# Kernel tuning notes

Hardware: AMD Instinct MI355X
Metric: run time of the kernel (lower is better)

The kernel has to match this reference:

```python
import jax, jax.numpy as jnp
import numpy as np

H = 1024
V = 32000
L = 15
B = 512


def setup_inputs() -> dict:
    key = jax.random.key(0)
    ks = jax.random.split(key, 16)
    s = 0.02
    return {
        "input_ids": jax.random.randint(ks[0], (B,), 0, V),
        "hidden": jax.random.normal(ks[1], (1, B, H), jnp.float32),
        "encoder_outputs": jax.random.normal(ks[2], (L, B, H), jnp.float32),
        "max_length": L,
        "embedding": jax.random.normal(ks[3], (V, H), jnp.float32) * s,
        "attn1_w": jax.random.normal(ks[4], (1, 2 * H), jnp.float32) * s,
        "attn1_b": jnp.zeros((1,), jnp.float32),
        "combine_w": jax.random.normal(ks[5], (H, 2 * H), jnp.float32) * s,
        "combine_b": jnp.zeros((H,), jnp.float32),
        "w_ih": jax.random.normal(ks[6], (3 * H, H), jnp.float32) * s,
        "w_hh": jax.random.normal(ks[7], (3 * H, H), jnp.float32) * s,
        "b_ih": jnp.zeros((3 * H,), jnp.float32),
        "b_hh": jnp.zeros((3 * H,), jnp.float32),
        "out_w": jax.random.normal(ks[8], (V, H), jnp.float32) * s,
        "out_b": jnp.zeros((V,), jnp.float32),
    }


def reference(input_ids, hidden, encoder_outputs, max_length, embedding,
              attn1_w, attn1_b, combine_w, combine_b,
              w_ih, w_hh, b_ih, b_hh, out_w, out_b):
    # embedding lookup (dropout is identity in eval mode)
    emb = embedding[input_ids]                       # [B, H]
    # Bahdanau-style additive scores: vectorize the per-step python loop
    emb_l = jnp.broadcast_to(emb[None], (max_length, B, H))   # [L, B, H]
    cat = jnp.concatenate([emb_l, encoder_outputs], axis=-1)  # [L, B, 2H]
    scores = cat @ attn1_w.T + attn1_b               # [L, B, 1]
    attn_weights = jax.nn.softmax(scores, axis=0)    # softmax over L
    ctx = jnp.sum(attn_weights * encoder_outputs, axis=0)     # [B, H]
    x = jnp.concatenate([emb, ctx], axis=-1) @ combine_w.T + combine_b  # [B, H]
    # n_layers = 1: relu then one GRU step (seq len 1)
    x = jax.nn.relu(x)
    h = hidden[0]                                    # [B, H]
    gi = x @ w_ih.T + b_ih                           # [B, 3H]
    gh = h @ w_hh.T + b_hh                           # [B, 3H]
    i_r, i_z, i_n = jnp.split(gi, 3, axis=1)
    h_r, h_z, h_n = jnp.split(gh, 3, axis=1)
    r = jax.nn.sigmoid(i_r + h_r)
    z = jax.nn.sigmoid(i_z + h_z)
    n = jnp.tanh(i_n + r * h_n)
    h_new = (1.0 - z) * n + z * h                    # [B, H]
    logits = h_new @ out_w.T + out_b                 # [B, V]
    output = jax.nn.log_softmax(logits, axis=1)
    return output, h_new[None], attn_weights
```

## Files before the change

kernel.cpp:

```cpp
#include <hip/hip_runtime.h>

#define HH 1024
#define VV 32000
#define LL 15
#define BB 512

typedef __bf16 bf16;
typedef __bf16 bf16x4 __attribute__((ext_vector_type(4)));
typedef __bf16 bf16x8 __attribute__((ext_vector_type(8)));
typedef float f32x4 __attribute__((ext_vector_type(4)));

__device__ __forceinline__ unsigned short f2bf(float f) {
    unsigned int u = __float_as_uint(f);
    unsigned int r = (u + 0x7fffu + ((u >> 16) & 1u)) >> 16;
    return (unsigned short)r;
}

__device__ __forceinline__ void gld_lds16(const void* g, void* l) {
    __builtin_amdgcn_global_load_lds(
        (const __attribute__((address_space(1))) unsigned int*)g,
        (__attribute__((address_space(3))) unsigned int*)l, 16, 0, 0);
}

__global__ __launch_bounds__(256)
void cvt4_kernel(const float* __restrict__ a0, unsigned short* __restrict__ o0, int n0_,
                 const float* __restrict__ a1, unsigned short* __restrict__ o1, int n1_,
                 const float* __restrict__ a2, unsigned short* __restrict__ o2, int n2_,
                 const float* __restrict__ a3, unsigned short* __restrict__ o3, int n3_) {
    int i = blockIdx.x * 256 + threadIdx.x;
    const float* src; unsigned short* dst;
    if (i < n0_) { src = a0; dst = o0; }
    else if ((i -= n0_) < n1_) { src = a1; dst = o1; }
    else if ((i -= n1_) < n2_) { src = a2; dst = o2; }
    else if ((i -= n2_) < n3_) { src = a3; dst = o3; }
    else return;
    const f32x4 a = ((const f32x4*)src)[2 * i], b = ((const f32x4*)src)[2 * i + 1];
    ((bf16x4*)dst)[2 * i]     = __builtin_convertvector(a, bf16x4);
    ((bf16x4*)dst)[2 * i + 1] = __builtin_convertvector(b, bf16x4);
}

__global__ __launch_bounds__(256)
void attn_kernel(const int* __restrict__ ids, const float* __restrict__ enc,
                 const float* __restrict__ embedding,
                 const float* __restrict__ attn1_w, const float* __restrict__ attn1_b,
                 float* __restrict__ attn_out, unsigned short* __restrict__ cat_out) {
    const int b = blockIdx.x, tid = threadIdx.x;
    const int lane = tid & 63, wv = tid >> 6;

    __shared__ float s_enc[LL * HH];
    __shared__ float s_scores[LL];
    __shared__ float s_red[4];

    for (int idx = tid; idx < LL * HH / 4; idx += 256) {
        const int l = (idx * 4) >> 10, h = (idx * 4) & (HH - 1);
        *(f32x4*)&s_enc[idx * 4] = *(const f32x4*)&enc[((size_t)l * BB + b) * HH + h];
    }

    const float* embr = embedding + (size_t)ids[b] * HH;
    float p = 0.f;
    for (int j = tid; j < HH; j += 256) p += embr[j] * attn1_w[j];
    #pragma unroll
    for (int o = 32; o; o >>= 1) p += __shfl_xor(p, o);
    if (lane == 0) s_red[wv] = p;
    __syncthreads();
    const float semb = s_red[0] + s_red[1] + s_red[2] + s_red[3] + attn1_b[0];

    for (int l = wv; l < LL; l += 4) {
        float q = 0.f;
        for (int j = lane; j < HH; j += 64) q += s_enc[l * HH + j] * attn1_w[HH + j];
        #pragma unroll
        for (int o = 32; o; o >>= 1) q += __shfl_xor(q, o);
        if (lane == 0) s_scores[l] = q + semb;
    }
    __syncthreads();

    float mx = -3.4e38f;
    #pragma unroll
    for (int l = 0; l < LL; l++) mx = fmaxf(mx, s_scores[l]);
    float aw[LL], sum = 0.f;
    #pragma unroll
    for (int l = 0; l < LL; l++) { aw[l] = __expf(s_scores[l] - mx); sum += aw[l]; }
    const float inv = 1.f / sum;
    #pragma unroll
    for (int l = 0; l < LL; l++) aw[l] *= inv;

    if (tid < LL) attn_out[tid * BB + b] = aw[tid];

    for (int j = tid; j < HH; j += 256) {
        float c = 0.f;
        #pragma unroll
        for (int l = 0; l < LL; l++) c += aw[l] * s_enc[l * HH + j];
        cat_out[(size_t)b * (2 * HH) + j] = f2bf(embr[j]);
        cat_out[(size_t)b * (2 * HH) + HH + j] = f2bf(c);
    }
}

template<int TM, int TN, int OUT, int GATES>
__global__ __launch_bounds__(256)
void gemm_nt(const bf16* __restrict__ A, const bf16* __restrict__ B,
             const float* __restrict__ bias, void* __restrict__ Cout,
             const bf16* __restrict__ A2, const bf16* __restrict__ B2,
             const float* __restrict__ bias2, void* __restrict__ C2,
             const int K, const int N) {
    constexpr int FM = TM / 32, FN = TN / 32;
    __shared__ bf16 As[2][TM * 64];
    __shared__ bf16 Bs[2][TN * 64];

    if (GATES && blockIdx.z == 1) { A = A2; B = B2; bias = bias2; Cout = C2; }

    const int tid = threadIdx.x;
    const int lane = tid & 63, wave = tid >> 6;
    const int wm = wave >> 1, wn = wave & 1;
    const int rlo = lane & 15, khi = lane >> 4;
    const int m0 = blockIdx.y * TM, n0 = blockIdx.x * TN;

    f32x4 acc[FM][FN] = {};
    constexpr int IA = TM / 32, IB = TN / 32;

    auto stage = [&](int k0, int buf) {
        #pragma unroll
        for (int i = 0; i < IA; i++) {
            const int p = (i * 256 + tid) * 16;
            const int row = p >> 7;
            const int qs = (p & 127) ^ ((row & 7) << 4);
            gld_lds16(A + (size_t)(m0 + row) * K + k0 + (qs >> 1),
                      &As[buf][0] + i * 2048 + wave * 512);
        }
        #pragma unroll
        for (int i = 0; i < IB; i++) {
            const int p = (i * 256 + tid) * 16;
            const int row = p >> 7;
            const int qs = (p & 127) ^ ((row & 7) << 4);
            gld_lds16(B + (size_t)(n0 + row) * K + k0 + (qs >> 1),
                      &Bs[buf][0] + i * 2048 + wave * 512);
        }
    };

    auto compute = [&](int buf) {
        #pragma unroll
        for (int ks = 0; ks < 2; ks++) {
            bf16x8 af[FM], bfr[FN];
            #pragma unroll
            for (int m = 0; m < FM; m++) {
                const int r = wm * (TM / 2) + m * 16 + rlo;
                const int sw = (ks * 64 + khi * 16) ^ ((r & 7) << 4);
                af[m] = *(const bf16x8*)((const char*)&As[buf][0] + r * 128 + sw);
            }
            #pragma unroll
            for (int n = 0; n < FN; n++) {
                const int r = wn * (TN / 2) + n * 16 + rlo;
                const int sw = (ks * 64 + khi * 16) ^ ((r & 7) << 4);
                bfr[n] = *(const bf16x8*)((const char*)&Bs[buf][0] + r * 128 + sw);
            }
            #pragma unroll
            for (int m = 0; m < FM; m++)
                #pragma unroll
                for (int n = 0; n < FN; n++)
                    acc[m][n] = __builtin_amdgcn_mfma_f32_16x16x32_bf16(af[m], bfr[n], acc[m][n], 0, 0, 0);
        }
    };

    stage(0, 0);
    __syncthreads();
    int cur = 0;
    const int NT = K >> 6;
    for (int kt = 0; kt < NT; kt++) {
        if (kt + 1 < NT) stage((kt + 1) << 6, cur ^ 1);
        compute(cur);
        __syncthreads();
        cur ^= 1;
    }

    #pragma unroll
    for (int m = 0; m < FM; m++) {
        const int gr = m0 + wm * (TM / 2) + m * 16 + khi * 4;
        #pragma unroll
        for (int n = 0; n < FN; n++) {
            const int gc = n0 + wn * (TN / 2) + n * 16 + rlo;
            const float bv = bias[gc];
            #pragma unroll
            for (int j = 0; j < 4; j++) {
                float v = acc[m][n][j] + bv;
                if (OUT == 1) {
                    v = fmaxf(v, 0.f);
                    ((unsigned short*)Cout)[(size_t)(gr + j) * N + gc] = f2bf(v);
                } else {
                    ((float*)Cout)[(size_t)(gr + j) * N + gc] = v;
                }
            }
        }
    }
}

__global__ __launch_bounds__(256, 3)
void gemm_out(const bf16* __restrict__ A, const float* __restrict__ B,
              const float* __restrict__ bias, float* __restrict__ C,
              float* __restrict__ pmax, float* __restrict__ psum) {
    constexpr int K = HH, N = VV;
    __shared__ bf16 As[2][128 * 64];
    __shared__ bf16 Bs[2][64 * 64];
    __shared__ float sPm[2][128], sPs[2][128];

    const int tid = threadIdx.x;
    const int lane = tid & 63, wave = tid >> 6;
    const int wm = wave >> 1, wn = wave & 1;
    const int rlo = lane & 15, khi = lane >> 4;

    constexpr int gridN = VV / 64;
    constexpr int nFull = (gridN >> 3) << 5;
    const int bidx = blockIdx.x;
    int g, jm;
    if (bidx < nFull) { const int s = bidx >> 5, rem = bidx & 31; jm = rem >> 3; g = s * 8 + (rem & 7); }
    else { const int rem = bidx - nFull; constexpr int gleft = gridN & 7; g = (gridN & ~7) + rem % gleft; jm = rem / gleft; }
    const int n0 = g * 64, m0 = jm * 128;

    f32x4 acc[4][2] = {};
    f32x4 bvA[4], bvB[4];

    auto loadB = [&](int k0, f32x4* bv) {
        #pragma unroll
        for (int i = 0; i < 4; i++) {
            const int idx = i * 256 + tid;
            const int row = idx >> 4, c4 = idx & 15;
            bv[i] = *(const f32x4*)(B + (size_t)(n0 + row) * K + k0 + c4 * 4);
        }
    };
    auto stageA = [&](int k0, int buf) {
        #pragma unroll
        for (int i = 0; i < 4; i++) {
            const int p = (i * 256 + tid) * 16;
            const int row = p >> 7;
            const int qs = (p & 127) ^ ((row & 7) << 4);
            gld_lds16(A + (size_t)(m0 + row) * K + k0 + (qs >> 1),
                      &As[buf][0] + i * 2048 + wave * 512);
        }
    };
    auto writeB = [&](const f32x4* bv, int buf) {
        #pragma unroll
        for (int i = 0; i < 4; i++) {
            const int idx = i * 256 + tid;
            const int row = idx >> 4, c4 = idx & 15;
            bf16x4 w = __builtin_convertvector(bv[i], bf16x4);
            *(bf16x4*)((char*)&Bs[buf][0] + row * 128 + ((c4 * 8) ^ ((row & 7) << 4))) = w;
        }
    };
    auto compute = [&](int buf) {
        #pragma unroll
        for (int ks = 0; ks < 2; ks++) {
            bf16x8 af[4], bfr[2];
            #pragma unroll
            for (int m = 0; m < 4; m++) {
                const int r = wm * 64 + m * 16 + rlo;
                const int sw = (ks * 64 + khi * 16) ^ ((r & 7) << 4);
                af[m] = *(const bf16x8*)((const char*)&As[buf][0] + r * 128 + sw);
            }
            #pragma unroll
            for (int n = 0; n < 2; n++) {
                const int r = wn * 32 + n * 16 + rlo;
                const int sw = (ks * 64 + khi * 16) ^ ((r & 7) << 4);
                bfr[n] = *(const bf16x8*)((const char*)&Bs[buf][0] + r * 128 + sw);
            }
            #pragma unroll
            for (int m = 0; m < 4; m++)
                #pragma unroll
                for (int n = 0; n < 2; n++)
                    acc[m][n] = __builtin_amdgcn_mfma_f32_16x16x32_bf16(af[m], bfr[n], acc[m][n], 0, 0, 0);
        }
    };

    loadB(0, bvA);
    stageA(0, 0);
    writeB(bvA, 0);
    loadB(64, bvA);
    __syncthreads();

    int cur = 0;
    for (int kt = 0; kt < 16; kt += 2) {
        {
            const int k1 = (kt + 1) << 6, k2 = (kt + 2) << 6;
            if (k1 < K) stageA(k1, cur ^ 1);
            if (k2 < K) loadB(k2, bvB);
            compute(cur);
            if (k1 < K) writeB(bvA, cur ^ 1);
            __syncthreads();
            cur ^= 1;
        }
        {
            const int k2 = (kt + 2) << 6, k3 = (kt + 3) << 6;
            if (k2 < K) stageA(k2, cur ^ 1);
            if (k3 < K) loadB(k3, bvA);
            compute(cur);
            if (k2 < K) writeB(bvB, cur ^ 1);
            __syncthreads();
            cur ^= 1;
        }
    }

    float bvn[2];
    #pragma unroll
    for (int n = 0; n < 2; n++) bvn[n] = bias[n0 + wn * 32 + n * 16 + rlo];

    #pragma unroll
    for (int m = 0; m < 4; m++) {
        const int rbase = wm * 64 + m * 16 + khi * 4;
        #pragma unroll
        for (int j = 0; j < 4; j++) {
            const int gr = m0 + rbase + j;
            float v[2];
            #pragma unroll
            for (int n = 0; n < 2; n++) {
                v[n] = acc[m][n][j] + bvn[n];
                C[(size_t)gr * N + n0 + wn * 32 + n * 16 + rlo] = v[n];
            }
            float lm = fmaxf(v[0], v[1]);
            #pragma unroll
            for (int o = 8; o; o >>= 1) lm = fmaxf(lm, __shfl_xor(lm, o));
            float ls = __expf(v[0] - lm) + __expf(v[1] - lm);
            #pragma unroll
            for (int o = 8; o; o >>= 1) ls += __shfl_xor(ls, o);
            if (rlo == 0) { sPm[wn][rbase + j] = lm; sPs[wn][rbase + j] = ls; }
        }
    }
    __syncthreads();
    if (tid < 128) {
        const float ma = sPm[0][tid], mb = sPm[1][tid];
        const float M = fmaxf(ma, mb);
        const float S = sPs[0][tid] * __expf(ma - M) + sPs[1][tid] * __expf(mb - M);
        pmax[(size_t)(m0 + tid) * 512 + g] = M;
        psum[(size_t)(m0 + tid) * 512 + g] = S;
    }
}

__global__ __launch_bounds__(256)
void gru_kernel(const float* __restrict__ gi, const float* __restrict__ gh,
                const float* __restrict__ h, float* __restrict__ hnew,
                unsigned short* __restrict__ hnew_bf) {
    const int i = blockIdx.x * 256 + threadIdx.x;
    const int e = i * 4;
    const int b = e >> 10, j = e & (HH - 1);
    const size_t o = ((size_t)b * 3 * HH + j) / 4;
    const f32x4 ir = ((const f32x4*)gi)[o],          iz = ((const f32x4*)gi)[o + HH / 4],
                in_ = ((const f32x4*)gi)[o + 2 * HH / 4];
    const f32x4 hr = ((const f32x4*)gh)[o],          hz = ((const f32x4*)gh)[o + HH / 4],
                hn = ((const f32x4*)gh)[o + 2 * HH / 4];
    const f32x4 hv = ((const f32x4*)h)[i];
    f32x4 out;
    ushort4 ob;
    #pragma unroll
    for (int c = 0; c < 4; c++) {
        const float r = 1.f / (1.f + __expf(-(ir[c] + hr[c])));
        const float z = 1.f / (1.f + __expf(-(iz[c] + hz[c])));
        const float n = tanhf(in_[c] + r * hn[c]);
        const float v = (1.f - z) * n + z * hv[c];
        out[c] = v;
        ((unsigned short*)&ob)[c] = f2bf(v);
    }
    ((f32x4*)hnew)[i] = out;
    ((ushort4*)hnew_bf)[i] = ob;
}

__global__ __launch_bounds__(512)
void lsm_final(const float* __restrict__ pmax, const float* __restrict__ psum,
               float* __restrict__ logits) {
    const int b = blockIdx.x, tid = threadIdx.x;
    const int lane = tid & 63, wv = tid >> 6;
    __shared__ float sm[8], ss[8];

    float m = -3.4e38f, s = 0.f;
    if (tid < VV / 64) { m = pmax[(size_t)b * 512 + tid]; s = psum[(size_t)b * 512 + tid]; }
    #pragma unroll
    for (int o = 32; o; o >>= 1) {
        const float mo = __shfl_xor(m, o), so = __shfl_xor(s, o);
        const float nm = fmaxf(m, mo);
        s = s * __expf(m - nm) + so * __expf(mo - nm);
        m = nm;
    }
    if (lane == 0) { sm[wv] = m; ss[wv] = s; }
    __syncthreads();
    float M = sm[0], S;
    #pragma unroll
    for (int w = 1; w < 8; w++) M = fmaxf(M, sm[w]);
    S = ss[0] * __expf(sm[0] - M);
    #pragma unroll
    for (int w = 1; w < 8; w++) S += ss[w] * __expf(sm[w] - M);
    const float lse = M + __logf(S);

    float* row = logits + (size_t)b * VV;
    for (int j = tid; j < VV / 4; j += 512) {
        f32x4 v = ((const f32x4*)row)[j];
        v[0] -= lse; v[1] -= lse; v[2] -= lse; v[3] -= lse;
        ((f32x4*)row)[j] = v;
    }
}

extern "C" void kernel_launch(void* const* d_in, const int* in_sizes, int n_in,
                              void* d_out, int out_size, void* d_ws, size_t ws_size,
                              hipStream_t stream) {
    const int*   ids       = (const int*)d_in[0];
    const float* hidden    = (const float*)d_in[1];
    const float* enc       = (const float*)d_in[2];
    const float* embedding = (const float*)d_in[4];
    const float* attn1_w   = (const float*)d_in[5];
    const float* attn1_b   = (const float*)d_in[6];
    const float* combine_w = (const float*)d_in[7];
    const float* combine_b = (const float*)d_in[8];
    const float* w_ih      = (const float*)d_in[9];
    const float* w_hh      = (const float*)d_in[10];
    const float* b_ih      = (const float*)d_in[11];
    const float* b_hh      = (const float*)d_in[12];
    const float* out_w     = (const float*)d_in[13];
    const float* out_b     = (const float*)d_in[14];

    float* out_lsm = (float*)d_out;
    float* out_h   = out_lsm + (size_t)BB * VV;
    float* out_aw  = out_h + (size_t)BB * HH;

    char* w = (char*)d_ws;
    unsigned short* w_ih_bf  = (unsigned short*)w;   w += (size_t)3 * HH * HH * 2;
    unsigned short* w_hh_bf  = (unsigned short*)w;   w += (size_t)3 * HH * HH * 2;
    unsigned short* w_cb_bf  = (unsigned short*)w;   w += (size_t)2 * HH * HH * 2;
    unsigned short* cat_bf   = (unsigned short*)w;   w += (size_t)BB * 2 * HH * 2;
    unsigned short* x_bf     = (unsigned short*)w;   w += (size_t)BB * HH * 2;
    unsigned short* hid_bf   = (unsigned short*)w;   w += (size_t)BB * HH * 2;
    unsigned short* hnew_bf  = (unsigned short*)w;   w += (size_t)BB * HH * 2;
    float* gi   = (float*)w;                         w += (size_t)BB * 3 * HH * 4;
    float* gh   = (float*)w;                         w += (size_t)BB * 3 * HH * 4;
    float* pmax = (float*)w;                         w += (size_t)BB * 512 * 4;
    float* psum = (float*)w;                         w += (size_t)BB * 512 * 4;

    cvt4_kernel<<<(3 * HH * HH / 8 * 2 + 2 * HH * HH / 8 + BB * HH / 8) / 256, 256, 0, stream>>>(
        w_ih, w_ih_bf, 3 * HH * HH / 8,
        w_hh, w_hh_bf, 3 * HH * HH / 8,
        combine_w, w_cb_bf, 2 * HH * HH / 8,
        hidden, hid_bf, BB * HH / 8);

    attn_kernel<<<BB, 256, 0, stream>>>(ids, enc, embedding, attn1_w, attn1_b, out_aw, cat_bf);

    gemm_nt<64, 64, 1, 0><<<dim3(HH / 64, BB / 64), 256, 0, stream>>>(
        (const bf16*)cat_bf, (const bf16*)w_cb_bf, combine_b, x_bf,
        nullptr, nullptr, nullptr, nullptr, 2 * HH, HH);

    gemm_nt<64, 64, 0, 1><<<dim3(3 * HH / 64, BB / 64, 2), 256, 0, stream>>>(
        (const bf16*)hid_bf, (const bf16*)w_hh_bf, b_hh, gh,
        (const bf16*)x_bf, (const bf16*)w_ih_bf, b_ih, gi, HH, 3 * HH);

    gru_kernel<<<(BB * HH / 4) / 256, 256, 0, stream>>>(gi, gh, hidden, out_h, hnew_bf);

    gemm_out<<<(VV / 64) * 4, 256, 0, stream>>>(
        (const bf16*)hnew_bf, out_w, out_b, out_lsm, pmax, psum);

    lsm_final<<<BB, 512, 0, stream>>>(pmax, psum, out_lsm);
}
```

Baseline: 183.8 us.

## Use explicit vmcnt waits and raw barriers for deeper double-buffered GEMM pipelining

Both GEMM kernels replace __syncthreads-based double buffering with a two-stage prefetch. Stage k+2 is issued right after the compute on stage k, and the code waits with explicit s_waitcnt vmcnt counts plus raw s_barrier and sched_barrier fences. This lets global-to-LDS loads stay in flight across compute instead of draining every iteration. The risk is correctness and hazards: the vmcnt values must match exactly the number of outstanding loads per thread, and the loop now assumes an even tile count.

```diff
diff --git a/kernel.cpp b/kernel.cpp
--- a/kernel.cpp
+++ b/kernel.cpp
@@ -9,6 +9,11 @@
 typedef __bf16 bf16x4 __attribute__((ext_vector_type(4)));
 typedef __bf16 bf16x8 __attribute__((ext_vector_type(8)));
 typedef float f32x4 __attribute__((ext_vector_type(4)));
+
+#define VMCNT(n) asm volatile("s_waitcnt vmcnt(" #n ")" ::: "memory")
+#define LGKM0    asm volatile("s_waitcnt lgkmcnt(0)" ::: "memory")
+#define SBAR     __builtin_amdgcn_s_barrier()
+#define SCHED0   __builtin_amdgcn_sched_barrier(0)
 
 __device__ __forceinline__ unsigned short f2bf(float f) {
     unsigned int u = __float_as_uint(f);
@@ -160,15 +165,27 @@
         }
     };
 
+    const int NT = K >> 6;
     stage(0, 0);
-    __syncthreads();
-    int cur = 0;
-    const int NT = K >> 6;
-    for (int kt = 0; kt < NT; kt++) {
-        if (kt + 1 < NT) stage((kt + 1) << 6, cur ^ 1);
-        compute(cur);
-        __syncthreads();
-        cur ^= 1;
+    stage(64, 1);
+
+    for (int kt = 0; kt < NT; kt += 2) {
+        {
+            const int t = kt;
+            if (t + 1 < NT) { VMCNT(4); } else { VMCNT(0); }
+            SCHED0; SBAR; SCHED0;
+            compute(0);
+            SCHED0; SBAR; SCHED0;
+            if (t + 2 < NT) stage((t + 2) << 6, 0);
+        }
+        {
+            const int t = kt + 1;
+            if (t + 1 < NT) { VMCNT(4); } else { VMCNT(0); }
+            SCHED0; SBAR; SCHED0;
+            compute(1);
+            SCHED0; SBAR; SCHED0;
+            if (t + 2 < NT) stage((t + 2) << 6, 1);
+        }
     }
 
     #pragma unroll
@@ -215,7 +232,7 @@
     const int n0 = g * 64, m0 = jm * 128;
 
     f32x4 acc[4][2] = {};
-    f32x4 bvA[4], bvB[4];
+    f32x4 b0[4], b1[4];
 
     auto loadB = [&](int k0, f32x4* bv) {
         #pragma unroll
@@ -268,31 +285,34 @@
         }
     };
 
-    loadB(0, bvA);
+    constexpr int NT = K >> 6;
+    loadB(0, b0);
     stageA(0, 0);
-    writeB(bvA, 0);
-    loadB(64, bvA);
-    __syncthreads();
-
-    int cur = 0;
-    for (int kt = 0; kt < 16; kt += 2) {
+    VMCNT(4);
+    writeB(b0, 0);
+    loadB(64, b1);
+    stageA(64, 1);
+
+    for (int kt = 0; kt < NT; kt += 2) {
         {
-            const int k1 = (kt + 1) << 6, k2 = (kt + 2) << 6;
-            if (k1 < K) stageA(k1, cur ^ 1);
-            if (k2 < K) loadB(k2, bvB);
-            compute(cur);
-            if (k1 < K) writeB(bvA, cur ^ 1);
-            __syncthreads();
-            cur ^= 1;
+            const int t = kt;
+            if (t + 1 < NT) { VMCNT(8); } else { VMCNT(0); }
+            LGKM0;
+            SCHED0; SBAR; SCHED0;
+            compute(0);
+            SCHED0; SBAR; SCHED0;
+            if (t + 1 < NT) { VMCNT(4); writeB(b1, 1); }
+            if (t + 2 < NT) { loadB((t + 2) << 6, b0); stageA((t + 2) << 6, 0); }
         }
         {
-            const int k2 = (kt + 2) << 6, k3 = (kt + 3) << 6;
-            if (k2 < K) stageA(k2, cur ^ 1);
-            if (k3 < K) loadB(k3, bvA);
-            compute(cur);
-            if (k2 < K) writeB(bvB, cur ^ 1);
-            __syncthreads();
-            cur ^= 1;
+            const int t = kt + 1;
+            if (t + 1 < NT) { VMCNT(8); } else { VMCNT(0); }
+            LGKM0;
+            SCHED0; SBAR; SCHED0;
+            compute(1);
+            SCHED0; SBAR; SCHED0;
+            if (t + 1 < NT) { VMCNT(4); writeB(b0, 0); }
+            if (t + 2 < NT) { loadB((t + 2) << 6, b1); stageA((t + 2) << 6, 1); }
         }
     }
 
```

Result: no change. 182.7 us (-0.6%).
